# Performance work log

Hardware: AMD Instinct MI355X
Metric: run time of the kernel (lower is better)

The kernel has to match this reference:

```python
import jax, jax.numpy as jnp
import numpy as np

NB_LAYERS, KSIZE = 4, 5
DILATIONS = [1, 2, 4, 8]
NEG_SLOPE = 0.1
BN_EPS = 1e-5


def _cont_conv(times, feats, mask, dilation, p):
    """One ContConv1d layer: causal gather of time-diffs -> kernel MLP -> weighted aggregate + skip + BN."""
    k1W, k1b, k2W, k2b, k3W, k3b, skipW, skipb, gamma, beta = p
    bs, L, Cin = feats.shape
    Cout = skipW.shape[1]
    lags = jnp.arange(KSIZE) * dilation                    # (K,) include_zero_lag=True -> lag 0 included
    idx = jnp.arange(L)[None, :] - lags[:, None]           # (K, L) causal neighbor indices
    valid = idx >= 0
    idx_c = jnp.clip(idx, 0, L - 1)
    g_times = times[:, idx_c]                              # (bs, K, L)
    g_feats = feats[:, idx_c, :]                           # (bs, K, L, Cin)
    g_mask = (mask[:, idx_c] & valid[None] & mask[:, None, :]).astype(feats.dtype)
    dt = (times[:, None, :] - g_times) * g_mask            # (bs, K, L) zeroed where invalid
    # kernel MLP: scalar time-diff -> (Cin, Cout) mixing matrix
    h = jax.nn.leaky_relu(dt[..., None] @ k1W + k1b, NEG_SLOPE)
    h = jax.nn.leaky_relu(h @ k2W + k2b, NEG_SLOPE)
    kv = (h @ k3W + k3b).reshape(bs, KSIZE, L, Cin, Cout) * g_mask[..., None, None]
    out = jnp.einsum('bklc,bklcd->bld', g_feats, kv)       # aggregate over taps and input channels
    out = out + feats @ skipW + skipb                      # 1x1-conv skip connection
    mu = out.mean((0, 1))                                  # BatchNorm1d (training-mode batch stats)
    var = out.var((0, 1))
    return (out - mu) * jax.lax.rsqrt(var + BN_EPS) * gamma + beta


def _ccnn_forward(event_times, event_types, emb, k1W, k1b, k2W, k2b, k3W, k3b, skipW, skipb, gamma, beta):
    bs = event_times.shape[0]
    emb = emb.at[0].set(0.0)                               # padding_idx = 0
    times = jnp.concatenate([jnp.zeros((bs, 1), event_times.dtype), event_times], axis=1)
    bos = jnp.full((bs, 1), jnp.max(event_types) + 1, dtype=event_types.dtype)
    types = jnp.concatenate([bos, event_types], axis=1)
    mask = times != 0                                      # BOS (t=0) masked, as in the original
    enc = emb[types]                                       # (bs, L+1, C)
    for i in range(NB_LAYERS):
        p = (k1W[i], k1b[i], k2W[i], k2b[i], k3W[i], k3b[i], skipW[i], skipb[i], gamma[i], beta[i])
        enc = jax.nn.leaky_relu(_cont_conv(times, enc, mask, DILATIONS[i], p), NEG_SLOPE)
    return enc


def setup_inputs() -> dict:
    key = jax.random.key(0)
    ks = jax.random.split(key, 12)
    bs, L, C, H, num_types = 8, 2048, 32, 16, 100
    s = 0.05
    gaps = jax.random.uniform(ks[0], (bs, L)) * 0.1 + 0.01
    times = jnp.cumsum(gaps, axis=1)                       # strictly increasing positive event times
    types = jax.random.randint(ks[1], (bs, L), 0, num_types) + 1   # 1..num_types
    pad = jnp.arange(L) >= int(0.9 * L)
    times = jnp.where(pad[None, :], 0.0, times).astype(jnp.float32)
    types = jnp.where(pad[None, :], 0, types).astype(jnp.int32)
    return {
        'event_times': times,
        'event_types': types,
        'emb': jax.random.normal(ks[2], (num_types + 2, C)) * s,
        'k1W': jax.random.normal(ks[3], (NB_LAYERS, 1, H)) * s,
        'k1b': jnp.zeros((NB_LAYERS, H)),
        'k2W': jax.random.normal(ks[4], (NB_LAYERS, H, H)) * s,
        'k2b': jnp.zeros((NB_LAYERS, H)),
        'k3W': jax.random.normal(ks[5], (NB_LAYERS, H, C * C)) * s,
        'k3b': jnp.zeros((NB_LAYERS, C * C)),
        'skipW': jax.random.normal(ks[6], (NB_LAYERS, C, C)) * s,
        'skipb': jnp.zeros((NB_LAYERS, C)),
        'gamma': jnp.ones((NB_LAYERS, C)),
        'beta': jnp.zeros((NB_LAYERS, C)),
    }


def reference(event_times, event_types, emb, k1W, k1b, k2W, k2b, k3W, k3b, skipW, skipb, gamma, beta):
    return _ccnn_forward(event_times, event_types, emb, k1W, k1b, k2W, k2b, k3W, k3b, skipW, skipb, gamma, beta)
```

## Files before the change

kernel.cpp:

```cpp
#include <hip/hip_runtime.h>
#include <stdint.h>

#define NB_LAYERS 4
#define KSIZE 5
#define BSZ 8
#define LIN 2048
#define LSEQ 2049
#define CCH 32
#define HCH 16
#define MROWS (BSZ*LSEQ)
#define NTILES ((MROWS+15)/16)
#define KDIM 576
#define NEG 0.1f
#define BNEPS 1e-5f
#define CONVGRID 205
#define CONVBLK 320

typedef _Float16 h2v __attribute__((ext_vector_type(2)));
typedef _Float16 h8v __attribute__((ext_vector_type(8)));
typedef float    f4v __attribute__((ext_vector_type(4)));

union H8 { h8v v; h2v h[4]; };

static __device__ __forceinline__ h2v mkh2(float a, float b) {
  h2v r; r[0] = (_Float16)a; r[1] = (_Float16)b; return r;
}

template<int MODE>
__global__ __launch_bounds__(CONVBLK) void conv_kernel(
    const float* __restrict__ enc_in,
    const int*   __restrict__ types,
    const float* __restrict__ emb,
    float* __restrict__ enc_out,
    const float* __restrict__ etimes,
    const float* __restrict__ k1Wp, const float* __restrict__ k1bp,
    const float* __restrict__ k2Wp, const float* __restrict__ k2bp,
    const float* __restrict__ k3W, const float* __restrict__ k3b,
    const float* __restrict__ skipW,
    _Float16* __restrict__ Wt,
    const float* __restrict__ stats_prev,
    const float* __restrict__ partials_prev,
    float* __restrict__ stats_out,
    float* __restrict__ partials_out,
    float* __restrict__ stats_zero,
    const float* __restrict__ gamma_prev, const float* __restrict__ beta_prev,
    int dil)
{
  __shared__ h8v swh[(CONVBLK/64) * KSIZE * 16 * 2];
  __shared__ alignas(16) float sW[304];
  __shared__ float sst[64];
  __shared__ float sbn[64];

  const int tid  = threadIdx.x;
  const int lane = tid & 63;
  const int wv   = tid >> 6;
  const int m    = lane & 15;
  const int q    = lane >> 4;

  if (tid < 64) { sst[tid] = 0.f; sbn[tid] = 0.f; }
  if (tid < 16) { sW[tid] = k1Wp[tid]; sW[16 + tid] = k1bp[tid]; sW[32 + tid] = k2bp[tid]; }
  if (tid >= 64) sW[48 + tid - 64] = k2Wp[tid - 64];

  if (MODE == 0) {
    if (blockIdx.x == 0 && tid < 192) stats_zero[tid] = 0.f;
    int id2 = blockIdx.x * CONVBLK + tid;
    if (id2 < 3 * CCH * KDIM) {
      int layer = 1 + id2 / (CCH * KDIM);
      int rem = id2 % (CCH * KDIM);
      int n = rem / KDIM;
      int k = rem % KDIM;
      float val;
      if (k < 512)      { int h = k >> 5, c = k & 31; val = k3W[layer*16384 + h*1024 + c*32 + n]; }
      else if (k < 544) { int c = k - 512;            val = k3b[layer*1024 + c*32 + n]; }
      else              { int c = k - 544;            val = skipW[layer*1024 + c*32 + n]; }
      Wt[layer * (CCH * KDIM) + rem] = (_Float16)val;
    }
  }
  __syncthreads();

  if (MODE == 1 && partials_prev) {
    float v = 0.f;
#pragma unroll 8
    for (int i = tid; i < CONVGRID * 64; i += CONVBLK) v += partials_prev[i];
    atomicAdd(&sbn[tid & 63], v);
    __syncthreads();
  }

  float sc8[8], ob8[8];
  if (MODE == 1) {
    const float inv = 1.f / (float)MROWS;
#pragma unroll
    for (int j = 0; j < 8; j++) {
      int c = q * 8 + j;
      float s1 = partials_prev ? sbn[c]      : stats_prev[c];
      float s2 = partials_prev ? sbn[32 + c] : stats_prev[32 + c];
      float mu = s1 * inv;
      float var = s2 * inv - mu * mu;
      float sc = gamma_prev[c] * rsqrtf(var + BNEPS);
      sc8[j] = sc; ob8[j] = beta_prev[c] - mu * sc;
    }
  }

  const _Float16* wb0 = Wt + m * KDIM + q * 8;
  const _Float16* wb1 = Wt + (m + 16) * KDIM + q * 8;

  const int tile = blockIdx.x * (CONVBLK / 64) + wv;
  int row = tile * 16 + m;
  bool rvalid = row < MROWS;
  int rowc = min(row, MROWS - 1);
  int b = rowc / LSEQ, pos = rowc % LSEQ;
  float t_l = (pos == 0) ? 0.f : etimes[b * LIN + pos - 1];
  bool mask_l = rvalid && (t_l != 0.f);

  int bosv = 0;
  if (MODE == 0) {
    if (__ballot(pos == 0)) {
      const int4* tp = (const int4*)types;
      int mx = 0;
#pragma unroll 4
      for (int i = lane; i < (BSZ * LIN) / 4; i += 64) {
        int4 v = tp[i];
        mx = max(mx, max(max(v.x, v.y), max(v.z, v.w)));
      }
#pragma unroll
      for (int off = 32; off; off >>= 1) mx = max(mx, __shfl_xor(mx, off, 64));
      bosv = mx + 1;
    }
  }

  int jcs[KSIZE]; float tjv[KSIZE];
#pragma unroll
  for (int tap = 0; tap < KSIZE; tap++) {
    int j = pos - tap * dil;
    int jc = max(j, 0); jcs[tap] = jc;
    tjv[tap] = (jc == 0) ? 0.f : etimes[b * LIN + jc - 1];
  }
  float4 fa[KSIZE], fbv[KSIZE];
  int tts[KSIZE];
  if (MODE == 0) {
#pragma unroll
    for (int tap = 0; tap < KSIZE; tap++) {
      int jc = jcs[tap];
      tts[tap] = (jc > 0) ? types[b * LIN + jc - 1] : ((tap == 0) ? bosv : 0);
    }
#pragma unroll
    for (int tap = 0; tap < KSIZE; tap++) {
      const float* ep = emb + tts[tap] * CCH + q * 8;
      fa[tap] = *(const float4*)ep; fbv[tap] = *(const float4*)(ep + 4);
    }
  } else {
#pragma unroll
    for (int tap = 0; tap < KSIZE; tap++) {
      const float* fp = enc_in + (b * LSEQ + jcs[tap]) * CCH + q * 8;
      fa[tap] = *(const float4*)fp; fbv[tap] = *(const float4*)(fp + 4);
    }
  }

  h2v fh[KSIZE][4];
  h2v fself[4];
  float Fb[8];
#pragma unroll
  for (int jj = 0; jj < 8; jj++) Fb[jj] = 0.f;

#pragma unroll
  for (int tap = 0; tap < KSIZE; tap++) {
    bool gm = mask_l && (pos - tap * dil >= 0) && (tjv[tap] != 0.f);
    float fv[8] = {fa[tap].x, fa[tap].y, fa[tap].z, fa[tap].w,
                   fbv[tap].x, fbv[tap].y, fbv[tap].z, fbv[tap].w};
    if (MODE == 0) {
      float zf = (tts[tap] != 0) ? 1.f : 0.f;
#pragma unroll
      for (int jj = 0; jj < 8; jj++) fv[jj] *= zf;
    } else {
#pragma unroll
      for (int jj = 0; jj < 8; jj++) {
        float x = fmaf(fv[jj], sc8[jj], ob8[jj]);
        fv[jj] = fmaxf(x, NEG * x);
      }
    }
    if (tap == 0) {
      float rv = rvalid ? 1.f : 0.f;
#pragma unroll
      for (int p2 = 0; p2 < 4; p2++) fself[p2] = mkh2(fv[2*p2] * rv, fv[2*p2+1] * rv);
    }
    float g = gm ? 1.f : 0.f;
#pragma unroll
    for (int jj = 0; jj < 8; jj++) Fb[jj] += g * fv[jj];
#pragma unroll
    for (int p2 = 0; p2 < 4; p2++) fh[tap][p2] = mkh2(fv[2*p2], fv[2*p2+1]);
  }

#pragma unroll
  for (int rep = 0; rep < 2; rep++) {
    const int jt = rep ? (KSIZE - 1) : (lane >> 4);
    const bool act = rep ? (lane < 16) : true;
    int j2 = pos - jt * dil;
    int jc2 = max(j2, 0);
    float tj2 = (jc2 == 0) ? 0.f : etimes[b * LIN + jc2 - 1];
    bool g2 = act && mask_l && (j2 >= 0) && (tj2 != 0.f);
    float dt = g2 ? (t_l - tj2) : 0.f;

    H8 w0, w1;
    if (__ballot(g2)) {
      const f4v* k1wv = (const f4v*)&sW[0];
      const f4v* k1bv = (const f4v*)&sW[16];
      const f4v* k2bv = (const f4v*)&sW[32];
      float h1[HCH], h2[HCH];
#pragma unroll
      for (int h4 = 0; h4 < 4; h4++) {
        f4v cw = k1wv[h4], cb = k1bv[h4], c2 = k2bv[h4];
#pragma unroll
        for (int r = 0; r < 4; r++) {
          float x = fmaf(dt, cw[r], cb[r]);
          h1[h4*4+r] = fmaxf(x, NEG * x);
          h2[h4*4+r] = c2[r];
        }
      }
#pragma unroll
      for (int hp = 0; hp < HCH; hp++) {
        float hv = h1[hp];
        const f4v* kk = (const f4v*)&sW[48 + hp * 16];
#pragma unroll
        for (int h4 = 0; h4 < 4; h4++) {
          f4v c = kk[h4];
#pragma unroll
          for (int r = 0; r < 4; r++) h2[h4*4+r] = fmaf(hv, c[r], h2[h4*4+r]);
        }
      }
      float g = g2 ? 1.f : 0.f;
#pragma unroll
      for (int p2 = 0; p2 < 4; p2++) {
        float a0 = h2[2*p2];     a0 = fmaxf(a0, NEG * a0) * g;
        float a1 = h2[2*p2+1];   a1 = fmaxf(a1, NEG * a1) * g;
        w0.h[p2] = mkh2(a0, a1);
        float b0 = h2[8+2*p2];   b0 = fmaxf(b0, NEG * b0) * g;
        float b1 = h2[8+2*p2+1]; b1 = fmaxf(b1, NEG * b1) * g;
        w1.h[p2] = mkh2(b0, b1);
      }
    } else {
#pragma unroll
      for (int p2 = 0; p2 < 4; p2++) { w0.h[p2] = mkh2(0.f, 0.f); w1.h[p2] = mkh2(0.f, 0.f); }
    }
    if (act) {
      int base = ((wv * KSIZE + jt) * 16 + m) * 2;
      swh[base] = w0.v; swh[base + 1] = w1.v;
    }
  }
  __syncthreads();

  h2v wh[KSIZE][8];
#pragma unroll
  for (int tap = 0; tap < KSIZE; tap++) {
    int base = ((wv * KSIZE + tap) * 16 + m) * 2;
    H8 a0, a1; a0.v = swh[base]; a1.v = swh[base + 1];
#pragma unroll
    for (int p2 = 0; p2 < 4; p2++) { wh[tap][p2] = a0.h[p2]; wh[tap][4+p2] = a1.h[p2]; }
  }

  f4v aP = {0,0,0,0}, aQ = {0,0,0,0}, bP = {0,0,0,0}, bQ = {0,0,0,0};

#pragma unroll
  for (int ks = 0; ks < 16; ks++) {
    H8 bf0, bf1, af;
    if (MODE == 0) {
      const float* wp = k3W + ks * 1024 + (q * 8) * 32 + m;
#pragma unroll
      for (int p2 = 0; p2 < 4; p2++) {
        bf0.h[p2] = mkh2(wp[(2*p2) * 32],      wp[(2*p2+1) * 32]);
        bf1.h[p2] = mkh2(wp[(2*p2) * 32 + 16], wp[(2*p2+1) * 32 + 16]);
      }
    } else {
      bf0.v = *(const h8v*)(wb0 + ks * 32);
      bf1.v = *(const h8v*)(wb1 + ks * 32);
    }
    h2v u0 = mkh2(0.f,0.f), u1 = mkh2(0.f,0.f), u2 = mkh2(0.f,0.f), u3 = mkh2(0.f,0.f);
#pragma unroll
    for (int tap = 0; tap < KSIZE; tap++) {
      _Float16 w = wh[tap][ks >> 1][ks & 1];
      h2v wd; wd[0] = w; wd[1] = w;
      u0 += wd * fh[tap][0];
      u1 += wd * fh[tap][1];
      u2 += wd * fh[tap][2];
      u3 += wd * fh[tap][3];
    }
    af.h[0] = u0; af.h[1] = u1; af.h[2] = u2; af.h[3] = u3;
    if (ks & 1) {
      aQ = __builtin_amdgcn_mfma_f32_16x16x32_f16(af.v, bf0.v, aQ, 0, 0, 0);
      bQ = __builtin_amdgcn_mfma_f32_16x16x32_f16(af.v, bf1.v, bQ, 0, 0, 0);
    } else {
      aP = __builtin_amdgcn_mfma_f32_16x16x32_f16(af.v, bf0.v, aP, 0, 0, 0);
      bP = __builtin_amdgcn_mfma_f32_16x16x32_f16(af.v, bf1.v, bP, 0, 0, 0);
    }
  }
  {
    H8 bf0, bf1, af;
    if (MODE == 0) {
      const float* kp = k3b + (q * 8) * 32 + m;
#pragma unroll
      for (int p2 = 0; p2 < 4; p2++) {
        bf0.h[p2] = mkh2(kp[(2*p2) * 32],      kp[(2*p2+1) * 32]);
        bf1.h[p2] = mkh2(kp[(2*p2) * 32 + 16], kp[(2*p2+1) * 32 + 16]);
      }
    } else {
      bf0.v = *(const h8v*)(wb0 + 512);
      bf1.v = *(const h8v*)(wb1 + 512);
    }
#pragma unroll
    for (int p2 = 0; p2 < 4; p2++) af.h[p2] = mkh2(Fb[2*p2], Fb[2*p2+1]);
    aP = __builtin_amdgcn_mfma_f32_16x16x32_f16(af.v, bf0.v, aP, 0, 0, 0);
    bP = __builtin_amdgcn_mfma_f32_16x16x32_f16(af.v, bf1.v, bP, 0, 0, 0);
  }
  {
    H8 bf0, bf1, af;
    if (MODE == 0) {
      const float* sp = skipW + (q * 8) * 32 + m;
#pragma unroll
      for (int p2 = 0; p2 < 4; p2++) {
        bf0.h[p2] = mkh2(sp[(2*p2) * 32],      sp[(2*p2+1) * 32]);
        bf1.h[p2] = mkh2(sp[(2*p2) * 32 + 16], sp[(2*p2+1) * 32 + 16]);
      }
    } else {
      bf0.v = *(const h8v*)(wb0 + 544);
      bf1.v = *(const h8v*)(wb1 + 544);
    }
    af.h[0] = fself[0]; af.h[1] = fself[1]; af.h[2] = fself[2]; af.h[3] = fself[3];
    aQ = __builtin_amdgcn_mfma_f32_16x16x32_f16(af.v, bf0.v, aQ, 0, 0, 0);
    bQ = __builtin_amdgcn_mfma_f32_16x16x32_f16(af.v, bf1.v, bQ, 0, 0, 0);
  }
  f4v acc0 = aP + aQ;
  f4v acc1 = bP + bQ;

  float s0 = 0.f, s1 = 0.f, s2 = 0.f, s3 = 0.f;
#pragma unroll
  for (int r = 0; r < 4; r++) {
    float v0 = acc0[r], v1 = acc1[r];
    s0 += v0; s1 += v0 * v0; s2 += v1; s3 += v1 * v1;
    int rd = tile * 16 + q * 4 + r;
    if (rd < MROWS) {
      enc_out[rd * CCH + m] = v0;
      enc_out[rd * CCH + 16 + m] = v1;
    }
  }
  s0 += __shfl_xor(s0, 16, 64); s0 += __shfl_xor(s0, 32, 64);
  s1 += __shfl_xor(s1, 16, 64); s1 += __shfl_xor(s1, 32, 64);
  s2 += __shfl_xor(s2, 16, 64); s2 += __shfl_xor(s2, 32, 64);
  s3 += __shfl_xor(s3, 16, 64); s3 += __shfl_xor(s3, 32, 64);
  if (q == 0) {
    atomicAdd(&sst[m], s0);
    atomicAdd(&sst[32 + m], s1);
    atomicAdd(&sst[16 + m], s2);
    atomicAdd(&sst[48 + m], s3);
  }
  __syncthreads();
  if (tid < 64) {
    if (MODE == 0) partials_out[blockIdx.x * 64 + tid] = sst[tid];
    else           atomicAdd(&stats_out[tid], sst[tid]);
  }
}

__global__ __launch_bounds__(256) void bn_kernel(
    const float* __restrict__ x, float* __restrict__ out,
    const float* __restrict__ stats,
    const float* __restrict__ gamma, const float* __restrict__ beta) {
  int id = blockIdx.x * blockDim.x + threadIdx.x;
  int c = id & 31;
  const float inv = 1.f / (float)MROWS;
  float mu = stats[c] * inv;
  float var = stats[32 + c] * inv - mu * mu;
  float sc = gamma[c] * rsqrtf(var + BNEPS);
  float v = fmaf(x[id], sc, beta[c] - mu * sc);
  out[id] = fmaxf(v, NEG * v);
}

extern "C" void kernel_launch(void* const* d_in, const int* in_sizes, int n_in,
                              void* d_out, int out_size, void* d_ws, size_t ws_size,
                              hipStream_t stream) {
  (void)in_sizes; (void)n_in; (void)out_size; (void)ws_size;
  const float* event_times = (const float*)d_in[0];
  const int*   event_types = (const int*)d_in[1];
  const float* emb   = (const float*)d_in[2];
  const float* k1W   = (const float*)d_in[3];
  const float* k1b   = (const float*)d_in[4];
  const float* k2W   = (const float*)d_in[5];
  const float* k2b   = (const float*)d_in[6];
  const float* k3W   = (const float*)d_in[7];
  const float* k3b   = (const float*)d_in[8];
  const float* skipW = (const float*)d_in[9];
  const float* gamma = (const float*)d_in[11];
  const float* beta  = (const float*)d_in[12];

  float* enc_a = (float*)d_ws;
  float* enc_b = enc_a + (size_t)MROWS * CCH;
  float* stats = enc_b + (size_t)MROWS * CCH;
  float* partials0 = stats + NB_LAYERS * 64;
  _Float16* Wt = (_Float16*)(((uintptr_t)(partials0 + CONVGRID * 64) + 255) & ~(uintptr_t)255);

  conv_kernel<0><<<CONVGRID, CONVBLK, 0, stream>>>(
      nullptr, event_types, emb, enc_b, event_times,
      k1W, k1b, k2W, k2b, k3W, k3b, skipW, Wt,
      nullptr, nullptr, nullptr, partials0, stats + 64,
      nullptr, nullptr, 1);

  conv_kernel<1><<<CONVGRID, CONVBLK, 0, stream>>>(
      enc_b, nullptr, nullptr, enc_a, event_times,
      k1W + HCH, k1b + HCH, k2W + HCH*HCH, k2b + HCH,
      nullptr, nullptr, nullptr, Wt + 1 * CCH * KDIM,
      nullptr, partials0, stats + 64, nullptr, nullptr,
      gamma + 0 * CCH, beta + 0 * CCH, 2);

  conv_kernel<1><<<CONVGRID, CONVBLK, 0, stream>>>(
      enc_a, nullptr, nullptr, enc_b, event_times,
      k1W + 2*HCH, k1b + 2*HCH, k2W + 2*HCH*HCH, k2b + 2*HCH,
      nullptr, nullptr, nullptr, Wt + 2 * CCH * KDIM,
      stats + 64, nullptr, stats + 128, nullptr, nullptr,
      gamma + 1 * CCH, beta + 1 * CCH, 4);

  conv_kernel<1><<<CONVGRID, CONVBLK, 0, stream>>>(
      enc_b, nullptr, nullptr, enc_a, event_times,
      k1W + 3*HCH, k1b + 3*HCH, k2W + 3*HCH*HCH, k2b + 3*HCH,
      nullptr, nullptr, nullptr, Wt + 3 * CCH * KDIM,
      stats + 128, nullptr, stats + 192, nullptr, nullptr,
      gamma + 2 * CCH, beta + 2 * CCH, 8);

  bn_kernel<<<2049, 256, 0, stream>>>(enc_a, (float*)d_out,
      stats + 192, gamma + 3 * CCH, beta + 3 * CCH);
}
```

Baseline: 152.7 us.

## Pre-swizzle kernel weights into MFMA fragment order and enlarge conv blocks

The pre-transposed fp16 weight buffer for layers 1–3 is now stored in MFMA B-fragment order. Each lane loads its 8 halves with one contiguous, coalesced 16-byte access, replacing row-strided reads. The conv kernel moves from 320-thread to 512-thread blocks with a smaller grid, and adds a dead-tile path that still matches the barrier count. The final BN+LeakyReLU kernel becomes a float4 grid-stride loop with per-thread precomputed scale and offset. The trade-off is a few idle waves per launch and different occupancy from the larger blocks.

```diff
diff --git a/kernel.cpp b/kernel.cpp
--- a/kernel.cpp
+++ b/kernel.cpp
@@ -10,11 +10,12 @@
 #define HCH 16
 #define MROWS (BSZ*LSEQ)
 #define NTILES ((MROWS+15)/16)
-#define KDIM 576
 #define NEG 0.1f
 #define BNEPS 1e-5f
-#define CONVGRID 205
-#define CONVBLK 320
+#define CONVGRID 129
+#define CONVBLK 512
+#define NFRAG 36
+#define WT_HALVES (NFRAG*64*8)
 
 typedef _Float16 h2v __attribute__((ext_vector_type(2)));
 typedef _Float16 h8v __attribute__((ext_vector_type(8)));
@@ -24,6 +25,18 @@
 
 static __device__ __forceinline__ h2v mkh2(float a, float b) {
   h2v r; r[0] = (_Float16)a; r[1] = (_Float16)b; return r;
+}
+
+static __device__ __forceinline__ void wt_decode(
+    int g, const float* __restrict__ k3Wl, const float* __restrict__ k3bl,
+    const float* __restrict__ skipWl, int& halfidx, float& val) {
+  int n, k;
+  if (g < 16384)      { n = g & 31; int c = (g >> 5) & 31; int h = g >> 10; k = h * 32 + c; val = k3Wl[g]; }
+  else if (g < 17408) { int g2 = g - 16384; n = g2 & 31; int c = g2 >> 5; k = 512 + c; val = k3bl[g2]; }
+  else                { int g2 = g - 17408; n = g2 & 31; int c = g2 >> 5; k = 544 + c; val = skipWl[g2]; }
+  int m = n & 15, a = n >> 4, qq = (k >> 3) & 3, hh = k & 7;
+  int f = (k < 512) ? ((k >> 5) * 2 + a) : ((k < 544) ? (32 + a) : (34 + a));
+  halfidx = f * 512 + ((qq << 4) | m) * 8 + hh;
 }
 
 template<int MODE>
@@ -59,28 +72,24 @@
 
   if (tid < 64) { sst[tid] = 0.f; sbn[tid] = 0.f; }
   if (tid < 16) { sW[tid] = k1Wp[tid]; sW[16 + tid] = k1bp[tid]; sW[32 + tid] = k2bp[tid]; }
-  if (tid >= 64) sW[48 + tid - 64] = k2Wp[tid - 64];
+  if (tid >= 64 && tid < 320) sW[48 + tid - 64] = k2Wp[tid - 64];
 
   if (MODE == 0) {
     if (blockIdx.x == 0 && tid < 192) stats_zero[tid] = 0.f;
     int id2 = blockIdx.x * CONVBLK + tid;
-    if (id2 < 3 * CCH * KDIM) {
-      int layer = 1 + id2 / (CCH * KDIM);
-      int rem = id2 % (CCH * KDIM);
-      int n = rem / KDIM;
-      int k = rem % KDIM;
-      float val;
-      if (k < 512)      { int h = k >> 5, c = k & 31; val = k3W[layer*16384 + h*1024 + c*32 + n]; }
-      else if (k < 544) { int c = k - 512;            val = k3b[layer*1024 + c*32 + n]; }
-      else              { int c = k - 544;            val = skipW[layer*1024 + c*32 + n]; }
-      Wt[layer * (CCH * KDIM) + rem] = (_Float16)val;
+    if (id2 < 3 * WT_HALVES) {
+      int layer = 1 + id2 / WT_HALVES;
+      int g = id2 - (layer - 1) * WT_HALVES;
+      int hi; float val;
+      wt_decode(g, k3W + layer * 16384, k3b + layer * 1024, skipW + layer * 1024, hi, val);
+      Wt[(layer - 1) * WT_HALVES + hi] = (_Float16)val;
     }
   }
   __syncthreads();
 
   if (MODE == 1 && partials_prev) {
     float v = 0.f;
-#pragma unroll 8
+#pragma unroll 4
     for (int i = tid; i < CONVGRID * 64; i += CONVBLK) v += partials_prev[i];
     atomicAdd(&sbn[tid & 63], v);
     __syncthreads();
@@ -101,255 +110,258 @@
     }
   }
 
-  const _Float16* wb0 = Wt + m * KDIM + q * 8;
-  const _Float16* wb1 = Wt + (m + 16) * KDIM + q * 8;
-
   const int tile = blockIdx.x * (CONVBLK / 64) + wv;
-  int row = tile * 16 + m;
-  bool rvalid = row < MROWS;
-  int rowc = min(row, MROWS - 1);
-  int b = rowc / LSEQ, pos = rowc % LSEQ;
-  float t_l = (pos == 0) ? 0.f : etimes[b * LIN + pos - 1];
-  bool mask_l = rvalid && (t_l != 0.f);
-
-  int bosv = 0;
-  if (MODE == 0) {
-    if (__ballot(pos == 0)) {
-      const int4* tp = (const int4*)types;
-      int mx = 0;
+  const bool deadtile = (tile >= NTILES);
+
+  if (!deadtile) {
+    int row = tile * 16 + m;
+    bool rvalid = row < MROWS;
+    int rowc = min(row, MROWS - 1);
+    int b = rowc / LSEQ, pos = rowc % LSEQ;
+    float t_l = (pos == 0) ? 0.f : etimes[b * LIN + pos - 1];
+    bool mask_l = rvalid && (t_l != 0.f);
+
+    int bosv = 0;
+    if (MODE == 0) {
+      if (__ballot(pos == 0)) {
+        const int4* tp = (const int4*)types;
+        int mx = 0;
 #pragma unroll 4
-      for (int i = lane; i < (BSZ * LIN) / 4; i += 64) {
-        int4 v = tp[i];
-        mx = max(mx, max(max(v.x, v.y), max(v.z, v.w)));
-      }
-#pragma unroll
-      for (int off = 32; off; off >>= 1) mx = max(mx, __shfl_xor(mx, off, 64));
-      bosv = mx + 1;
-    }
-  }
-
-  int jcs[KSIZE]; float tjv[KSIZE];
-#pragma unroll
-  for (int tap = 0; tap < KSIZE; tap++) {
-    int j = pos - tap * dil;
-    int jc = max(j, 0); jcs[tap] = jc;
-    tjv[tap] = (jc == 0) ? 0.f : etimes[b * LIN + jc - 1];
-  }
-  float4 fa[KSIZE], fbv[KSIZE];
-  int tts[KSIZE];
-  if (MODE == 0) {
+        for (int i = lane; i < (BSZ * LIN) / 4; i += 64) {
+          int4 v = tp[i];
+          mx = max(mx, max(max(v.x, v.y), max(v.z, v.w)));
+        }
+#pragma unroll
+        for (int off = 32; off; off >>= 1) mx = max(mx, __shfl_xor(mx, off, 64));
+        bosv = mx + 1;
+      }
+    }
+
+    int jcs[KSIZE]; float tjv[KSIZE];
 #pragma unroll
     for (int tap = 0; tap < KSIZE; tap++) {
-      int jc = jcs[tap];
-      tts[tap] = (jc > 0) ? types[b * LIN + jc - 1] : ((tap == 0) ? bosv : 0);
-    }
+      int j = pos - tap * dil;
+      int jc = max(j, 0); jcs[tap] = jc;
+      tjv[tap] = (jc == 0) ? 0.f : etimes[b * LIN + jc - 1];
+    }
+    float4 fa[KSIZE], fbv[KSIZE];
+    int tts[KSIZE];
+    if (MODE == 0) {
+#pragma unroll
+      for (int tap = 0; tap < KSIZE; tap++) {
+        int jc = jcs[tap];
+        tts[tap] = (jc > 0) ? types[b * LIN + jc - 1] : ((tap == 0) ? bosv : 0);
+      }
+#pragma unroll
+      for (int tap = 0; tap < KSIZE; tap++) {
+        const float* ep = emb + tts[tap] * CCH + q * 8;
+        fa[tap] = *(const float4*)ep; fbv[tap] = *(const float4*)(ep + 4);
+      }
+    } else {
+#pragma unroll
+      for (int tap = 0; tap < KSIZE; tap++) {
+        const float* fp = enc_in + (b * LSEQ + jcs[tap]) * CCH + q * 8;
+        fa[tap] = *(const float4*)fp; fbv[tap] = *(const float4*)(fp + 4);
+      }
+    }
+
+    h2v fh[KSIZE][4];
+    h2v fself[4];
+    float Fb[8];
+#pragma unroll
+    for (int jj = 0; jj < 8; jj++) Fb[jj] = 0.f;
+
 #pragma unroll
     for (int tap = 0; tap < KSIZE; tap++) {
-      const float* ep = emb + tts[tap] * CCH + q * 8;
-      fa[tap] = *(const float4*)ep; fbv[tap] = *(const float4*)(ep + 4);
-    }
-  } else {
+      bool gm = mask_l && (pos - tap * dil >= 0) && (tjv[tap] != 0.f);
+      float fv[8] = {fa[tap].x, fa[tap].y, fa[tap].z, fa[tap].w,
+                     fbv[tap].x, fbv[tap].y, fbv[tap].z, fbv[tap].w};
+      if (MODE == 0) {
+        float zf = (tts[tap] != 0) ? 1.f : 0.f;
+#pragma unroll
+        for (int jj = 0; jj < 8; jj++) fv[jj] *= zf;
+      } else {
+#pragma unroll
+        for (int jj = 0; jj < 8; jj++) {
+          float x = fmaf(fv[jj], sc8[jj], ob8[jj]);
+          fv[jj] = fmaxf(x, NEG * x);
+        }
+      }
+      if (tap == 0) {
+        float rv = rvalid ? 1.f : 0.f;
+#pragma unroll
+        for (int p2 = 0; p2 < 4; p2++) fself[p2] = mkh2(fv[2*p2] * rv, fv[2*p2+1] * rv);
+      }
+      float g = gm ? 1.f : 0.f;
+#pragma unroll
+      for (int jj = 0; jj < 8; jj++) Fb[jj] += g * fv[jj];
+#pragma unroll
+      for (int p2 = 0; p2 < 4; p2++) fh[tap][p2] = mkh2(fv[2*p2], fv[2*p2+1]);
+    }
+
+#pragma unroll
+    for (int rep = 0; rep < 2; rep++) {
+      const int jt = rep ? (KSIZE - 1) : (lane >> 4);
+      const bool act = rep ? (lane < 16) : true;
+      int j2 = pos - jt * dil;
+      int jc2 = max(j2, 0);
+      float tj2 = (jc2 == 0) ? 0.f : etimes[b * LIN + jc2 - 1];
+      bool g2 = act && mask_l && (j2 >= 0) && (tj2 != 0.f);
+      float dt = g2 ? (t_l - tj2) : 0.f;
+
+      H8 w0, w1;
+      if (__ballot(g2)) {
+        const f4v* k1wv = (const f4v*)&sW[0];
+        const f4v* k1bv = (const f4v*)&sW[16];
+        const f4v* k2bv = (const f4v*)&sW[32];
+        float h1[HCH], h2[HCH];
+#pragma unroll
+        for (int h4 = 0; h4 < 4; h4++) {
+          f4v cw = k1wv[h4], cb = k1bv[h4], c2 = k2bv[h4];
+#pragma unroll
+          for (int r = 0; r < 4; r++) {
+            float x = fmaf(dt, cw[r], cb[r]);
+            h1[h4*4+r] = fmaxf(x, NEG * x);
+            h2[h4*4+r] = c2[r];
+          }
+        }
+#pragma unroll
+        for (int hp = 0; hp < HCH; hp++) {
+          float hv = h1[hp];
+          const f4v* kk = (const f4v*)&sW[48 + hp * 16];
+#pragma unroll
+          for (int h4 = 0; h4 < 4; h4++) {
+            f4v c = kk[h4];
+#pragma unroll
+            for (int r = 0; r < 4; r++) h2[h4*4+r] = fmaf(hv, c[r], h2[h4*4+r]);
+          }
+        }
+        float g = g2 ? 1.f : 0.f;
+#pragma unroll
+        for (int p2 = 0; p2 < 4; p2++) {
+          float a0 = h2[2*p2];     a0 = fmaxf(a0, NEG * a0) * g;
+          float a1 = h2[2*p2+1];   a1 = fmaxf(a1, NEG * a1) * g;
+          w0.h[p2] = mkh2(a0, a1);
+          float b0 = h2[8+2*p2];   b0 = fmaxf(b0, NEG * b0) * g;
+          float b1 = h2[8+2*p2+1]; b1 = fmaxf(b1, NEG * b1) * g;
+          w1.h[p2] = mkh2(b0, b1);
+        }
+      } else {
+#pragma unroll
+        for (int p2 = 0; p2 < 4; p2++) { w0.h[p2] = mkh2(0.f, 0.f); w1.h[p2] = mkh2(0.f, 0.f); }
+      }
+      if (act) {
+        int base = ((wv * KSIZE + jt) * 16 + m) * 2;
+        swh[base] = w0.v; swh[base + 1] = w1.v;
+      }
+    }
+    __syncthreads();
+
+    h2v wh[KSIZE][8];
 #pragma unroll
     for (int tap = 0; tap < KSIZE; tap++) {
-      const float* fp = enc_in + (b * LSEQ + jcs[tap]) * CCH + q * 8;
-      fa[tap] = *(const float4*)fp; fbv[tap] = *(const float4*)(fp + 4);
-    }
-  }
-
-  h2v fh[KSIZE][4];
-  h2v fself[4];
-  float Fb[8];
-#pragma unroll
-  for (int jj = 0; jj < 8; jj++) Fb[jj] = 0.f;
-
-#pragma unroll
-  for (int tap = 0; tap < KSIZE; tap++) {
-    bool gm = mask_l && (pos - tap * dil >= 0) && (tjv[tap] != 0.f);
-    float fv[8] = {fa[tap].x, fa[tap].y, fa[tap].z, fa[tap].w,
-                   fbv[tap].x, fbv[tap].y, fbv[tap].z, fbv[tap].w};
-    if (MODE == 0) {
-      float zf = (tts[tap] != 0) ? 1.f : 0.f;
-#pragma unroll
-      for (int jj = 0; jj < 8; jj++) fv[jj] *= zf;
-    } else {
-#pragma unroll
-      for (int jj = 0; jj < 8; jj++) {
-        float x = fmaf(fv[jj], sc8[jj], ob8[jj]);
-        fv[jj] = fmaxf(x, NEG * x);
-      }
-    }
-    if (tap == 0) {
-      float rv = rvalid ? 1.f : 0.f;
-#pragma unroll
-      for (int p2 = 0; p2 < 4; p2++) fself[p2] = mkh2(fv[2*p2] * rv, fv[2*p2+1] * rv);
-    }
-    float g = gm ? 1.f : 0.f;
-#pragma unroll
-    for (int jj = 0; jj < 8; jj++) Fb[jj] += g * fv[jj];
-#pragma unroll
-    for (int p2 = 0; p2 < 4; p2++) fh[tap][p2] = mkh2(fv[2*p2], fv[2*p2+1]);
-  }
-
-#pragma unroll
-  for (int rep = 0; rep < 2; rep++) {
-    const int jt = rep ? (KSIZE - 1) : (lane >> 4);
-    const bool act = rep ? (lane < 16) : true;
-    int j2 = pos - jt * dil;
-    int jc2 = max(j2, 0);
-    float tj2 = (jc2 == 0) ? 0.f : etimes[b * LIN + jc2 - 1];
-    bool g2 = act && mask_l && (j2 >= 0) && (tj2 != 0.f);
-    float dt = g2 ? (t_l - tj2) : 0.f;
-
-    H8 w0, w1;
-    if (__ballot(g2)) {
-      const f4v* k1wv = (const f4v*)&sW[0];
-      const f4v* k1bv = (const f4v*)&sW[16];
-      const f4v* k2bv = (const f4v*)&sW[32];
-      float h1[HCH], h2[HCH];
-#pragma unroll
-      for (int h4 = 0; h4 < 4; h4++) {
-        f4v cw = k1wv[h4], cb = k1bv[h4], c2 = k2bv[h4];
-#pragma unroll
-        for (int r = 0; r < 4; r++) {
-          float x = fmaf(dt, cw[r], cb[r]);
-          h1[h4*4+r] = fmaxf(x, NEG * x);
-          h2[h4*4+r] = c2[r];
-        }
-      }
-#pragma unroll
-      for (int hp = 0; hp < HCH; hp++) {
-        float hv = h1[hp];
-        const f4v* kk = (const f4v*)&sW[48 + hp * 16];
-#pragma unroll
-        for (int h4 = 0; h4 < 4; h4++) {
-          f4v c = kk[h4];
-#pragma unroll
-          for (int r = 0; r < 4; r++) h2[h4*4+r] = fmaf(hv, c[r], h2[h4*4+r]);
-        }
-      }
-      float g = g2 ? 1.f : 0.f;
-#pragma unroll
-      for (int p2 = 0; p2 < 4; p2++) {
-        float a0 = h2[2*p2];     a0 = fmaxf(a0, NEG * a0) * g;
-        float a1 = h2[2*p2+1];   a1 = fmaxf(a1, NEG * a1) * g;
-        w0.h[p2] = mkh2(a0, a1);
-        float b0 = h2[8+2*p2];   b0 = fmaxf(b0, NEG * b0) * g;
-        float b1 = h2[8+2*p2+1]; b1 = fmaxf(b1, NEG * b1) * g;
-        w1.h[p2] = mkh2(b0, b1);
-      }
-    } else {
-#pragma unroll
-      for (int p2 = 0; p2 < 4; p2++) { w0.h[p2] = mkh2(0.f, 0.f); w1.h[p2] = mkh2(0.f, 0.f); }
-    }
-    if (act) {
-      int base = ((wv * KSIZE + jt) * 16 + m) * 2;
-      swh[base] = w0.v; swh[base + 1] = w1.v;
-    }
-  }
-  __syncthreads();
-
-  h2v wh[KSIZE][8];
-#pragma unroll
-  for (int tap = 0; tap < KSIZE; tap++) {
-    int base = ((wv * KSIZE + tap) * 16 + m) * 2;
-    H8 a0, a1; a0.v = swh[base]; a1.v = swh[base + 1];
-#pragma unroll
-    for (int p2 = 0; p2 < 4; p2++) { wh[tap][p2] = a0.h[p2]; wh[tap][4+p2] = a1.h[p2]; }
-  }
-
-  f4v aP = {0,0,0,0}, aQ = {0,0,0,0}, bP = {0,0,0,0}, bQ = {0,0,0,0};
-
-#pragma unroll
-  for (int ks = 0; ks < 16; ks++) {
-    H8 bf0, bf1, af;
-    if (MODE == 0) {
-      const float* wp = k3W + ks * 1024 + (q * 8) * 32 + m;
-#pragma unroll
-      for (int p2 = 0; p2 < 4; p2++) {
-        bf0.h[p2] = mkh2(wp[(2*p2) * 32],      wp[(2*p2+1) * 32]);
-        bf1.h[p2] = mkh2(wp[(2*p2) * 32 + 16], wp[(2*p2+1) * 32 + 16]);
-      }
-    } else {
-      bf0.v = *(const h8v*)(wb0 + ks * 32);
-      bf1.v = *(const h8v*)(wb1 + ks * 32);
-    }
-    h2v u0 = mkh2(0.f,0.f), u1 = mkh2(0.f,0.f), u2 = mkh2(0.f,0.f), u3 = mkh2(0.f,0.f);
-#pragma unroll
-    for (int tap = 0; tap < KSIZE; tap++) {
-      _Float16 w = wh[tap][ks >> 1][ks & 1];
-      h2v wd; wd[0] = w; wd[1] = w;
-      u0 += wd * fh[tap][0];
-      u1 += wd * fh[tap][1];
-      u2 += wd * fh[tap][2];
-      u3 += wd * fh[tap][3];
-    }
-    af.h[0] = u0; af.h[1] = u1; af.h[2] = u2; af.h[3] = u3;
-    if (ks & 1) {
+      int base = ((wv * KSIZE + tap) * 16 + m) * 2;
+      H8 a0, a1; a0.v = swh[base]; a1.v = swh[base + 1];
+#pragma unroll
+      for (int p2 = 0; p2 < 4; p2++) { wh[tap][p2] = a0.h[p2]; wh[tap][4+p2] = a1.h[p2]; }
+    }
+
+    f4v aP = {0,0,0,0}, aQ = {0,0,0,0}, bP = {0,0,0,0}, bQ = {0,0,0,0};
+
+#pragma unroll
+    for (int ks = 0; ks < 16; ks++) {
+      H8 bf0, bf1, af;
+      if (MODE == 0) {
+        const float* wp = k3W + ks * 1024 + (q * 8) * 32 + m;
+#pragma unroll
+        for (int p2 = 0; p2 < 4; p2++) {
+          bf0.h[p2] = mkh2(wp[(2*p2) * 32],      wp[(2*p2+1) * 32]);
+          bf1.h[p2] = mkh2(wp[(2*p2) * 32 + 16], wp[(2*p2+1) * 32 + 16]);
+        }
+      } else {
+        bf0.v = *(const h8v*)(Wt + (size_t)((2*ks + 0) * 64 + lane) * 8);
+        bf1.v = *(const h8v*)(Wt + (size_t)((2*ks + 1) * 64 + lane) * 8);
+      }
+      h2v u0 = mkh2(0.f,0.f), u1 = mkh2(0.f,0.f), u2 = mkh2(0.f,0.f), u3 = mkh2(0.f,0.f);
+#pragma unroll
+      for (int tap = 0; tap < KSIZE; tap++) {
+        _Float16 w = wh[tap][ks >> 1][ks & 1];
+        h2v wd; wd[0] = w; wd[1] = w;
+        u0 += wd * fh[tap][0];
+        u1 += wd * fh[tap][1];
+        u2 += wd * fh[tap][2];
+        u3 += wd * fh[tap][3];
+      }
+      af.h[0] = u0; af.h[1] = u1; af.h[2] = u2; af.h[3] = u3;
+      if (ks & 1) {
+        aQ = __builtin_amdgcn_mfma_f32_16x16x32_f16(af.v, bf0.v, aQ, 0, 0, 0);
+        bQ = __builtin_amdgcn_mfma_f32_16x16x32_f16(af.v, bf1.v, bQ, 0, 0, 0);
+      } else {
+        aP = __builtin_amdgcn_mfma_f32_16x16x32_f16(af.v, bf0.v, aP, 0, 0, 0);
+        bP = __builtin_amdgcn_mfma_f32_16x16x32_f16(af.v, bf1.v, bP, 0, 0, 0);
+      }
+    }
+    {
+      H8 bf0, bf1, af;
+      if (MODE == 0) {
+        const float* kp = k3b + (q * 8) * 32 + m;
+#pragma unroll
+        for (int p2 = 0; p2 < 4; p2++) {
+          bf0.h[p2] = mkh2(kp[(2*p2) * 32],      kp[(2*p2+1) * 32]);
+          bf1.h[p2] = mkh2(kp[(2*p2) * 32 + 16], kp[(2*p2+1) * 32 + 16]);
+        }
+      } else {
+        bf0.v = *(const h8v*)(Wt + (size_t)(32 * 64 + lane) * 8);
+        bf1.v = *(const h8v*)(Wt + (size_t)(33 * 64 + lane) * 8);
+      }
+#pragma unroll
+      for (int p2 = 0; p2 < 4; p2++) af.h[p2] = mkh2(Fb[2*p2], Fb[2*p2+1]);
+      aP = __builtin_amdgcn_mfma_f32_16x16x32_f16(af.v, bf0.v, aP, 0, 0, 0);
+      bP = __builtin_amdgcn_mfma_f32_16x16x32_f16(af.v, bf1.v, bP, 0, 0, 0);
+    }
+    {
+      H8 bf0, bf1, af;
+      if (MODE == 0) {
+        const float* sp = skipW + (q * 8) * 32 + m;
+#pragma unroll
+        for (int p2 = 0; p2 < 4; p2++) {
+          bf0.h[p2] = mkh2(sp[(2*p2) * 32],      sp[(2*p2+1) * 32]);
+          bf1.h[p2] = mkh2(sp[(2*p2) * 32 + 16], sp[(2*p2+1) * 32 + 16]);
+        }
+      } else {
+        bf0.v = *(const h8v*)(Wt + (size_t)(34 * 64 + lane) * 8);
+        bf1.v = *(const h8v*)(Wt + (size_t)(35 * 64 + lane) * 8);
+      }
+      af.h[0] = fself[0]; af.h[1] = fself[1]; af.h[2] = fself[2]; af.h[3] = fself[3];
       aQ = __builtin_amdgcn_mfma_f32_16x16x32_f16(af.v, bf0.v, aQ, 0, 0, 0);
       bQ = __builtin_amdgcn_mfma_f32_16x16x32_f16(af.v, bf1.v, bQ, 0, 0, 0);
-    } else {
-      aP = __builtin_amdgcn_mfma_f32_16x16x32_f16(af.v, bf0.v, aP, 0, 0, 0);
-      bP = __builtin_amdgcn_mfma_f32_16x16x32_f16(af.v, bf1.v, bP, 0, 0, 0);
-    }
-  }
-  {
-    H8 bf0, bf1, af;
-    if (MODE == 0) {
-      const float* kp = k3b + (q * 8) * 32 + m;
-#pragma unroll
-      for (int p2 = 0; p2 < 4; p2++) {
-        bf0.h[p2] = mkh2(kp[(2*p2) * 32],      kp[(2*p2+1) * 32]);
-        bf1.h[p2] = mkh2(kp[(2*p2) * 32 + 16], kp[(2*p2+1) * 32 + 16]);
-      }
-    } else {
-      bf0.v = *(const h8v*)(wb0 + 512);
-      bf1.v = *(const h8v*)(wb1 + 512);
-    }
-#pragma unroll
-    for (int p2 = 0; p2 < 4; p2++) af.h[p2] = mkh2(Fb[2*p2], Fb[2*p2+1]);
-    aP = __builtin_amdgcn_mfma_f32_16x16x32_f16(af.v, bf0.v, aP, 0, 0, 0);
-    bP = __builtin_amdgcn_mfma_f32_16x16x32_f16(af.v, bf1.v, bP, 0, 0, 0);
-  }
-  {
-    H8 bf0, bf1, af;
-    if (MODE == 0) {
-      const float* sp = skipW + (q * 8) * 32 + m;
-#pragma unroll
-      for (int p2 = 0; p2 < 4; p2++) {
-        bf0.h[p2] = mkh2(sp[(2*p2) * 32],      sp[(2*p2+1) * 32]);
-        bf1.h[p2] = mkh2(sp[(2*p2) * 32 + 16], sp[(2*p2+1) * 32 + 16]);
-      }
-    } else {
-      bf0.v = *(const h8v*)(wb0 + 544);
-      bf1.v = *(const h8v*)(wb1 + 544);
-    }
-    af.h[0] = fself[0]; af.h[1] = fself[1]; af.h[2] = fself[2]; af.h[3] = fself[3];
-    aQ = __builtin_amdgcn_mfma_f32_16x16x32_f16(af.v, bf0.v, aQ, 0, 0, 0);
-    bQ = __builtin_amdgcn_mfma_f32_16x16x32_f16(af.v, bf1.v, bQ, 0, 0, 0);
-  }
-  f4v acc0 = aP + aQ;
-  f4v acc1 = bP + bQ;
-
-  float s0 = 0.f, s1 = 0.f, s2 = 0.f, s3 = 0.f;
-#pragma unroll
-  for (int r = 0; r < 4; r++) {
-    float v0 = acc0[r], v1 = acc1[r];
-    s0 += v0; s1 += v0 * v0; s2 += v1; s3 += v1 * v1;
-    int rd = tile * 16 + q * 4 + r;
-    if (rd < MROWS) {
-      enc_out[rd * CCH + m] = v0;
-      enc_out[rd * CCH + 16 + m] = v1;
-    }
-  }
-  s0 += __shfl_xor(s0, 16, 64); s0 += __shfl_xor(s0, 32, 64);
-  s1 += __shfl_xor(s1, 16, 64); s1 += __shfl_xor(s1, 32, 64);
-  s2 += __shfl_xor(s2, 16, 64); s2 += __shfl_xor(s2, 32, 64);
-  s3 += __shfl_xor(s3, 16, 64); s3 += __shfl_xor(s3, 32, 64);
-  if (q == 0) {
-    atomicAdd(&sst[m], s0);
-    atomicAdd(&sst[32 + m], s1);
-    atomicAdd(&sst[16 + m], s2);
-    atomicAdd(&sst[48 + m], s3);
+    }
+    f4v acc0 = aP + aQ;
+    f4v acc1 = bP + bQ;
+
+    float s0 = 0.f, s1 = 0.f, s2 = 0.f, s3 = 0.f;
+#pragma unroll
+    for (int r = 0; r < 4; r++) {
+      float v0 = acc0[r], v1 = acc1[r];
+      s0 += v0; s1 += v0 * v0; s2 += v1; s3 += v1 * v1;
+      int rd = tile * 16 + q * 4 + r;
+      if (rd < MROWS) {
+        enc_out[rd * CCH + m] = v0;
+        enc_out[rd * CCH + 16 + m] = v1;
+      }
+    }
+    s0 += __shfl_xor(s0, 16, 64); s0 += __shfl_xor(s0, 32, 64);
+    s1 += __shfl_xor(s1, 16, 64); s1 += __shfl_xor(s1, 32, 64);
+    s2 += __shfl_xor(s2, 16, 64); s2 += __shfl_xor(s2, 32, 64);
+    s3 += __shfl_xor(s3, 16, 64); s3 += __shfl_xor(s3, 32, 64);
+    if (q == 0) {
+      atomicAdd(&sst[m], s0);
+      atomicAdd(&sst[32 + m], s1);
+      atomicAdd(&sst[16 + m], s2);
+      atomicAdd(&sst[48 + m], s3);
+    }
+  } else {
+    __syncthreads();
   }
   __syncthreads();
   if (tid < 64) {
@@ -362,14 +374,27 @@
     const float* __restrict__ x, float* __restrict__ out,
     const float* __restrict__ stats,
     const float* __restrict__ gamma, const float* __restrict__ beta) {
-  int id = blockIdx.x * blockDim.x + threadIdx.x;
-  int c = id & 31;
+  int idx0 = blockIdx.x * 256 + threadIdx.x;
+  int c0 = (idx0 * 4) & 31;
   const float inv = 1.f / (float)MROWS;
-  float mu = stats[c] * inv;
-  float var = stats[32 + c] * inv - mu * mu;
-  float sc = gamma[c] * rsqrtf(var + BNEPS);
-  float v = fmaf(x[id], sc, beta[c] - mu * sc);
-  out[id] = fmaxf(v, NEG * v);
+  float sc[4], ob[4];
+#pragma unroll
+  for (int r = 0; r < 4; r++) {
+    int c = c0 + r;
+    float mu = stats[c] * inv;
+    float var = stats[32 + c] * inv - mu * mu;
+    sc[r] = gamma[c] * rsqrtf(var + BNEPS);
+    ob[r] = beta[c] - mu * sc[r];
+  }
+  for (int i = idx0; i < (MROWS * CCH) / 4; i += 256 * 256) {
+    float4 v = ((const float4*)x)[i];
+    float4 o;
+    o.x = fmaf(v.x, sc[0], ob[0]); o.x = fmaxf(o.x, NEG * o.x);
+    o.y = fmaf(v.y, sc[1], ob[1]); o.y = fmaxf(o.y, NEG * o.y);
+    o.z = fmaf(v.z, sc[2], ob[2]); o.z = fmaxf(o.z, NEG * o.z);
+    o.w = fmaf(v.w, sc[3], ob[3]); o.w = fmaxf(o.w, NEG * o.w);
+    ((float4*)out)[i] = o;
+  }
 }
 
 extern "C" void kernel_launch(void* const* d_in, const int* in_sizes, int n_in,
@@ -404,24 +429,24 @@
   conv_kernel<1><<<CONVGRID, CONVBLK, 0, stream>>>(
       enc_b, nullptr, nullptr, enc_a, event_times,
       k1W + HCH, k1b + HCH, k2W + HCH*HCH, k2b + HCH,
-      nullptr, nullptr, nullptr, Wt + 1 * CCH * KDIM,
+      nullptr, nullptr, nullptr, Wt + 0 * WT_HALVES,
       nullptr, partials0, stats + 64, nullptr, nullptr,
       gamma + 0 * CCH, beta + 0 * CCH, 2);
 
   conv_kernel<1><<<CONVGRID, CONVBLK, 0, stream>>>(
       enc_a, nullptr, nullptr, enc_b, event_times,
       k1W + 2*HCH, k1b + 2*HCH, k2W + 2*HCH*HCH, k2b + 2*HCH,
-      nullptr, nullptr, nullptr, Wt + 2 * CCH * KDIM,
+      nullptr, nullptr, nullptr, Wt + 1 * WT_HALVES,
       stats + 64, nullptr, stats + 128, nullptr, nullptr,
       gamma + 1 * CCH, beta + 1 * CCH, 4);
 
   conv_kernel<1><<<CONVGRID, CONVBLK, 0, stream>>>(
       enc_b, nullptr, nullptr, enc_a, event_times,
       k1W + 3*HCH, k1b + 3*HCH, k2W + 3*HCH*HCH, k2b + 3*HCH,
-      nullptr, nullptr, nullptr, Wt + 3 * CCH * KDIM,
+      nullptr, nullptr, nullptr, Wt + 2 * WT_HALVES,
       stats + 128, nullptr, stats + 192, nullptr, nullptr,
       gamma + 2 * CCH, beta + 2 * CCH, 8);
 
-  bn_kernel<<<2049, 256, 0, stream>>>(enc_a, (float*)d_out,
+  bn_kernel<<<256, 256, 0, stream>>>(enc_a, (float*)d_out,
       stats + 192, gamma + 3 * CCH, beta + 3 * CCH);
 }
```

New measurement: 149.9 us. Within noise of the previous version (-1.9%).
